# Kernel tuning notes

Hardware: AMD Instinct MI355X
Metric: run time of the kernel (lower is better)

Reference implementation:

```python
import jax, jax.numpy as jnp
import numpy as np

CHANNELS = 512
KSIZE = 5


def conv1d(x, w, b, pad):
    # x: (B, Cin, T), w: (Cout, Cin, k) -> (B, Cout, T)
    y = jax.lax.conv_general_dilated(
        x, w, window_strides=(1,), padding=[(pad, pad)],
        dimension_numbers=('NCH', 'OIH', 'NCH'))
    return y + b[None, :, None]


def setup_inputs() -> dict:
    key = jax.random.key(0)
    ks = jax.random.split(key, 10)
    B, C, T, K = 16, CHANNELS, 2048, KSIZE
    s = 0.02  # conv init scale
    return {
        'x': jax.random.normal(ks[0], (B, C, T), jnp.float32),
        'offset_w': jax.random.normal(ks[1], (2 * K, C, 3), jnp.float32) * s,
        'offset_b': jnp.zeros((2 * K,), jnp.float32),
        'mod_w': jax.random.normal(ks[2], (K, C, 3), jnp.float32) * s,
        'mod_b': jnp.zeros((K,), jnp.float32),
        'weight': jax.random.normal(ks[3], (C, C, K), jnp.float32),
        'rp1_w': jax.random.normal(ks[4], (C // 2, C, 3), jnp.float32) * s,
        'rp1_b': jnp.zeros((C // 2,), jnp.float32),
        'rp2_w': jax.random.normal(ks[5], (1, C // 2, 1), jnp.float32) * s,
        'rp2_b': jnp.zeros((1,), jnp.float32),
    }


def deformable_conv1d(x, offset, modulator, weight):
    B, C, T = x.shape
    K = weight.shape[-1]
    # offset: (B, 2K, T) -> (B, T, 2, K); only component 0 is used (as in torch src)
    off = offset.reshape(B, 2, K, T).transpose(0, 3, 1, 2)[:, :, 0, :]   # (B, T, K)
    mod = modulator.reshape(B, K, T).transpose(0, 2, 1)                   # (B, T, K)
    base = jnp.arange(T, dtype=x.dtype)[None, :, None]
    kpos = (jnp.arange(K, dtype=x.dtype) - K // 2)[None, None, :]
    pos = jnp.clip(base + kpos + off, 0, T - 1)                           # (B, T, K)
    pf = jnp.clip(jnp.floor(pos).astype(jnp.int32), 0, T - 1)
    pc = jnp.clip(jnp.ceil(pos).astype(jnp.int32), 0, T - 1)
    wf = pc.astype(x.dtype) - pos    # NB: both weights are 0 at integer pos (faithful to source)
    wc = pos - pf.astype(x.dtype)
    # gather along time for all channels at once: (B, C, T, K)
    sf = jnp.take_along_axis(x, pf.reshape(B, 1, T * K), axis=2).reshape(B, C, T, K)
    sc = jnp.take_along_axis(x, pc.reshape(B, 1, T * K), axis=2).reshape(B, C, T, K)
    sampled = sf * wf[:, None] + sc * wc[:, None]
    # only diagonal weight[c, c, k] is used in the source loops
    wdiag = weight[jnp.arange(C), jnp.arange(C), :]                       # (C, K)
    return jnp.einsum('bctk,ck,btk->bct', sampled, wdiag, mod)


def reference(x, offset_w, offset_b, mod_w, mod_b, weight, rp1_w, rp1_b, rp2_w, rp2_b):
    offset = conv1d(x, offset_w, offset_b, pad=1)            # (B, 2K, T)
    modulator = jax.nn.sigmoid(conv1d(x, mod_w, mod_b, pad=1))  # (B, K, T)
    deformed = deformable_conv1d(x, offset, modulator, weight)  # (B, C, T)
    h = jax.nn.relu(conv1d(deformed, rp1_w, rp1_b, pad=1))
    strength = conv1d(h, rp2_w, rp2_b, pad=0)[:, 0, :]          # (B, T)
    return deformed, strength
```

## Files before the change

### kernel.cpp

```cpp
#include <hip/hip_runtime.h>
#include <hip/hip_bf16.h>

#define CHN 512
#define TLEN 2048
#define KSZ 5
#define BATCH 16

typedef __hip_bfloat16 bf16;
typedef short bf16x8 __attribute__((ext_vector_type(8)));
typedef float f32x4  __attribute__((ext_vector_type(4)));

#define SAMP_BYTES (BATCH*TLEN*KSZ*8)
#define W1T_ELEMS  (16*4*3*64*40)
#define W1T_BYTES  (W1T_ELEMS*2)
#define WPK_BYTES  65536
#define DT_ROWS    2050
#define DT_CHUNK   (DT_ROWS*32)
#define DT_BYTES   ((size_t)BATCH*16*DT_CHUNK*2)

__global__ __launch_bounds__(256) void kPrep(const float* __restrict__ w1,
    bf16* __restrict__ w1t, const float* __restrict__ ow,
    const float* __restrict__ mw, float* __restrict__ wpk,
    float* __restrict__ outs, const float* __restrict__ b2p,
    bf16* __restrict__ dt)
{
  int bx = blockIdx.x;
  int tidl = threadIdx.x;
  const int NP = W1T_ELEMS/256;
  if (bx < NP) {
    int idx  = bx*256 + tidl;
    int c40  = idx % 40;
    int rest = idx / 40;
    int row  = rest & 63;
    int rr   = rest >> 6;
    int r    = rr % 3;
    int cq   = rr / 3;
    int q    = cq & 3;
    int ch   = cq >> 2;
    int co   = q*64 + row;
    float v = 0.f;
    if (c40 < 32) v = w1[(size_t)co*(CHN*3) + (ch*32 + c40)*3 + r];
    w1t[idx] = __float2bfloat16(v);
  } else if (bx < NP + 64) {
    int idx = (bx - NP)*256 + tidl;
    int j = idx & 31, c = idx >> 5;
    float v = 0.f;
    if (j < 15)      { int o = j/3,  d = j - o*3;  v = ow[o*(CHN*3) + c*3 + d]; }
    else if (j < 30) { int jj = j-15; int o = jj/3, d = jj - o*3;
                       v = mw[o*(CHN*3) + c*3 + d]; }
    wpk[idx] = v;
  } else if (bx < NP + 192) {
    outs[(bx - NP - 64)*256 + tidl] = b2p[0];
  } else if (dt) {
    int z = (bx - NP - 192)*256 + tidl;
    int chunk = z >> 6;
    int row   = ((z >> 5) & 1) ? (DT_ROWS-1) : 0;
    int col   = z & 31;
    dt[(size_t)chunk*DT_CHUNK + row*32 + col] = __float2bfloat16(0.f);
  }
}

__global__ __launch_bounds__(512) void kS(const float* __restrict__ x,
    const float* __restrict__ wpk, const float* __restrict__ ob,
    const float* __restrict__ mb, float2* __restrict__ samp)
{
  int b  = blockIdx.y;
  int t0 = blockIdx.x*64;
  int tx = threadIdx.x;
  int cg = threadIdx.y;
  int t  = t0 + tx;

  __shared__ float red[8][64][10];

  float acc[10];
  #pragma unroll
  for (int i=0;i<10;++i) acc[i]=0.f;
  const float* xb = x + (size_t)b*CHN*TLEN;
  int c0 = cg*64;
  #pragma unroll 4
  for (int c=c0;c<c0+64;++c) {
    int cu = __builtin_amdgcn_readfirstlane(c);
    const float* wp = wpk + cu*32;
    const float* xr = xb + (size_t)cu*TLEN;
    float xm = (t>0)      ? xr[t-1] : 0.f;
    float xc = xr[t];
    float xp = (t<TLEN-1) ? xr[t+1] : 0.f;
    #pragma unroll
    for (int o=0;o<5;++o) {
      acc[o]   = fmaf(xm, wp[o*3+0],    acc[o]);
      acc[o]   = fmaf(xc, wp[o*3+1],    acc[o]);
      acc[o]   = fmaf(xp, wp[o*3+2],    acc[o]);
      acc[5+o] = fmaf(xm, wp[15+o*3+0], acc[5+o]);
      acc[5+o] = fmaf(xc, wp[15+o*3+1], acc[5+o]);
      acc[5+o] = fmaf(xp, wp[15+o*3+2], acc[5+o]);
    }
  }
  #pragma unroll
  for (int i=0;i<10;++i) red[cg][tx][i] = acc[i];
  __syncthreads();
  for (int s=4;s>0;s>>=1) {
    if (cg < s) {
      #pragma unroll
      for (int i=0;i<10;++i) red[cg][tx][i] += red[cg+s][tx][i];
    }
    __syncthreads();
  }
  if (cg==0) {
    #pragma unroll
    for (int k=0;k<KSZ;++k) {
      float off = red[0][tx][k]   + ob[k];
      float mv  = red[0][tx][5+k] + mb[k];
      float sig = 1.f/(1.f + expf(-mv));
      float pos = (float)(t + k - 2) + off;
      pos = fminf(fmaxf(pos, 0.f), (float)(TLEN-1));
      samp[((size_t)b*TLEN + t)*KSZ + k] = make_float2(pos, sig);
    }
  }
}

#define BT   128
#define HALO 16
#define XLEN 160

template<bool WDT>
__global__ __launch_bounds__(256) void kDf(const float* __restrict__ x,
    const float* __restrict__ wgt, const float2* __restrict__ sampg,
    float* __restrict__ out, bf16* __restrict__ dt)
{
  int b  = blockIdx.z;
  int c0 = blockIdx.y*64;
  int t0 = blockIdx.x*BT;
  int tx = threadIdx.x, cy = threadIdx.y;
  int tid = cy*64 + tx;

  __shared__ float  xs[64*XLEN];
  __shared__ float2 sp[BT*KSZ];
  __shared__ int okf;

  int lo = min(max(t0 - HALO, 0), TLEN - XLEN);

  if (tid == 0) okf = 1;
  for (int i = tid; i < BT*KSZ; i += 256)
    sp[i] = sampg[((size_t)b*TLEN + t0)*KSZ + i];

  const float* xb = x + (size_t)b*CHN*TLEN;
  #pragma unroll
  for (int it = 0; it < 10; ++it) {
    int idx = tid + it*256;
    int c  = idx / 40;
    int c4 = idx - c*40;
    const float* src = xb + (size_t)(c0 + c)*TLEN + lo + c4*4;
    __builtin_amdgcn_global_load_lds(
        (const __attribute__((address_space(1))) unsigned int*)src,
        (__attribute__((address_space(3))) unsigned int*)&xs[idx*4],
        16, 0, 0);
  }
  __syncthreads();

  int   bl[2][KSZ];
  float wf[2][KSZ], wc[2][KSZ];
  bool ok = true;
  #pragma unroll
  for (int j=0;j<2;++j)
    #pragma unroll
    for (int k=0;k<KSZ;++k) {
      float2 s = sp[(j*64+tx)*KSZ + k];
      float pos = s.x, sig = s.y;
      float pf = floorf(pos), pc = ceilf(pos);
      int base = min((int)pf, TLEN-2);
      wf[j][k] = (pc - pos)*sig;
      wc[j][k] = (pos - pf)*sig;
      int bloc = base - lo;
      bl[j][k] = bloc;
      ok = ok && (bloc >= 0) && (bloc <= XLEN-2);
    }
  if (!ok) okf = 0;
  __syncthreads();
  int fast = okf;

  unsigned pk0[8], pk1[8];
  if (fast) {
    #pragma unroll
    for (int i=0;i<16;++i) {
      int cl = cy*16 + i;
      int cu = __builtin_amdgcn_readfirstlane(c0 + cl);
      const float* wd = wgt + (size_t)cu*(CHN*KSZ) + (size_t)cu*KSZ;
      float w0 = wd[0], w1v = wd[1], w2v = wd[2], w3 = wd[3], w4 = wd[4];
      const float* xr = xs + cl*XLEN;
      float o0, o1;
      {
        float a = 0.f;
        a = fmaf(fmaf(xr[bl[0][0]+1], wc[0][0], xr[bl[0][0]]*wf[0][0]), w0,  a);
        a = fmaf(fmaf(xr[bl[0][1]+1], wc[0][1], xr[bl[0][1]]*wf[0][1]), w1v, a);
        a = fmaf(fmaf(xr[bl[0][2]+1], wc[0][2], xr[bl[0][2]]*wf[0][2]), w2v, a);
        a = fmaf(fmaf(xr[bl[0][3]+1], wc[0][3], xr[bl[0][3]]*wf[0][3]), w3,  a);
        a = fmaf(fmaf(xr[bl[0][4]+1], wc[0][4], xr[bl[0][4]]*wf[0][4]), w4,  a);
        o0 = a;
      }
      {
        float a = 0.f;
        a = fmaf(fmaf(xr[bl[1][0]+1], wc[1][0], xr[bl[1][0]]*wf[1][0]), w0,  a);
        a = fmaf(fmaf(xr[bl[1][1]+1], wc[1][1], xr[bl[1][1]]*wf[1][1]), w1v, a);
        a = fmaf(fmaf(xr[bl[1][2]+1], wc[1][2], xr[bl[1][2]]*wf[1][2]), w2v, a);
        a = fmaf(fmaf(xr[bl[1][3]+1], wc[1][3], xr[bl[1][3]]*wf[1][3]), w3,  a);
        a = fmaf(fmaf(xr[bl[1][4]+1], wc[1][4], xr[bl[1][4]]*wf[1][4]), w4,  a);
        o1 = a;
      }
      size_t op = ((size_t)b*CHN + cu)*TLEN + t0 + tx;
      out[op]      = o0;
      out[op + 64] = o1;
      if (WDT) {
        union { bf16 h; unsigned short u; } cv0, cv1;
        cv0.h = __float2bfloat16(o0);
        cv1.h = __float2bfloat16(o1);
        if (i & 1) { pk0[i>>1] |= (unsigned)cv0.u << 16;
                     pk1[i>>1] |= (unsigned)cv1.u << 16; }
        else       { pk0[i>>1]  = cv0.u;  pk1[i>>1]  = cv1.u; }
      }
    }
  } else {
    #pragma unroll
    for (int i=0;i<16;++i) {
      int cl = cy*16 + i;
      int cu = __builtin_amdgcn_readfirstlane(c0 + cl);
      const float* wd = wgt + (size_t)cu*(CHN*KSZ) + (size_t)cu*KSZ;
      float wk0 = wd[0], wk1 = wd[1], wk2 = wd[2], wk3 = wd[3], wk4 = wd[4];
      const float* xr = xb + (size_t)cu*TLEN + lo;
      float o[2];
      #pragma unroll
      for (int j=0;j<2;++j) {
        float a = 0.f;
        a = fmaf(fmaf(xr[bl[j][0]+1], wc[j][0], xr[bl[j][0]]*wf[j][0]), wk0, a);
        a = fmaf(fmaf(xr[bl[j][1]+1], wc[j][1], xr[bl[j][1]]*wf[j][1]), wk1, a);
        a = fmaf(fmaf(xr[bl[j][2]+1], wc[j][2], xr[bl[j][2]]*wf[j][2]), wk2, a);
        a = fmaf(fmaf(xr[bl[j][3]+1], wc[j][3], xr[bl[j][3]]*wf[j][3]), wk3, a);
        a = fmaf(fmaf(xr[bl[j][4]+1], wc[j][4], xr[bl[j][4]]*wf[j][4]), wk4, a);
        o[j] = a;
      }
      size_t op = ((size_t)b*CHN + cu)*TLEN + t0 + tx;
      out[op]      = o[0];
      out[op + 64] = o[1];
      if (WDT) {
        union { bf16 h; unsigned short u; } cv0, cv1;
        cv0.h = __float2bfloat16(o[0]);
        cv1.h = __float2bfloat16(o[1]);
        if (i & 1) { pk0[i>>1] |= (unsigned)cv0.u << 16;
                     pk1[i>>1] |= (unsigned)cv1.u << 16; }
        else       { pk0[i>>1]  = cv0.u;  pk1[i>>1]  = cv1.u; }
      }
    }
  }

  if (WDT) {
    int ch   = (c0 >> 5) + (cy >> 1);
    int colb = (cy & 1)*16;
    bf16* p0 = dt + (size_t)(b*16 + ch)*DT_CHUNK
                  + (size_t)(t0 + tx + 1)*32 + colb;
    *(uint4*)p0       = make_uint4(pk0[0], pk0[1], pk0[2], pk0[3]);
    *((uint4*)p0 + 1) = make_uint4(pk0[4], pk0[5], pk0[6], pk0[7]);
    bf16* p1 = p0 + 64*32;
    *(uint4*)p1       = make_uint4(pk1[0], pk1[1], pk1[2], pk1[3]);
    *((uint4*)p1 + 1) = make_uint4(pk1[4], pk1[5], pk1[6], pk1[7]);
  }
}

#define DMA_W2(dst, ch_) do {                                                  \
  const char* gs = (const char*)(w1t + (size_t)((ch_)*4 + m0)*7680);           \
  char* ld = (char*)&Ws[dst][0];                                               \
  for (int of = tid*16; of < 15360; of += 4096) {                              \
    __builtin_amdgcn_global_load_lds(                                          \
        (const __attribute__((address_space(1))) unsigned int*)(gs + of),      \
        (__attribute__((address_space(3))) unsigned int*)(ld + of), 16, 0, 0); \
  }                                                                            \
} while(0)

#define DMA_D2(dst, ch_) do {                                                  \
  const char* gs = (const char*)(dt + (size_t)(b*16 + (ch_))*DT_CHUNK          \
                                    + (size_t)t0*32);                          \
  char* ld = (char*)&Dt[dst][0];                                               \
  for (int of = tid*16; of < 16512; of += 4096) {                              \
    __builtin_amdgcn_global_load_lds(                                          \
        (const __attribute__((address_space(1))) unsigned int*)(gs + of),      \
        (__attribute__((address_space(3))) unsigned int*)(ld + of), 16, 0, 0); \
  }                                                                            \
} while(0)

#define COMPUTE2(cur) do {                                                     \
  _Pragma("unroll")                                                            \
  for (int r=0;r<3;++r) {                                                      \
    bf16x8 af[4], bfr[4];                                                      \
    _Pragma("unroll")                                                          \
    for (int mt=0;mt<4;++mt)                                                   \
      af[mt] = *(const bf16x8*)&Ws[cur][(size_t)(r*64 + mt*16 + ln15)*40 + quad*8];\
    _Pragma("unroll")                                                          \
    for (int nt=0;nt<4;++nt)                                                   \
      bfr[nt] = *(const bf16x8*)&Dt[cur][(size_t)(wN*64 + nt*16 + ln15 + r)*32 + quad*8];\
    _Pragma("unroll")                                                          \
    for (int mt=0;mt<4;++mt)                                                   \
      _Pragma("unroll")                                                        \
      for (int nt=0;nt<4;++nt)                                                 \
        acc[mt][nt] = __builtin_amdgcn_mfma_f32_16x16x32_bf16(                 \
            af[mt], bfr[nt], acc[mt][nt], 0, 0, 0);                            \
  }                                                                            \
} while(0)

__global__ __launch_bounds__(256, 2) void k2d(const bf16* __restrict__ dt,
    const bf16* __restrict__ w1t, const float* __restrict__ b1,
    const float* __restrict__ w2, float* __restrict__ outs)
{
  int n0 = blockIdx.x*256;
  int m0 = blockIdx.y;
  int b  = n0 / TLEN;
  int t0 = n0 % TLEN;
  int tid  = threadIdx.x;
  int lane = tid & 63;
  int wN   = tid >> 6;
  int ln15 = lane & 15, quad = lane >> 4;

  __shared__ bf16 Ws[2][3*64*40];
  __shared__ bf16 Dt[2][258*32];
  __shared__ float Ss[256];

  f32x4 acc[4][4];
  #pragma unroll
  for (int i=0;i<4;++i)
    #pragma unroll
    for (int j=0;j<4;++j) acc[i][j] = (f32x4){0.f,0.f,0.f,0.f};

  DMA_W2(0, 0);
  DMA_D2(0, 0);
  __syncthreads();

  for (int ch=0; ch<16; ++ch) {
    int cur = ch & 1;
    int nxt = cur ^ 1;
    if (ch < 15) {
      DMA_W2(nxt, ch+1);
      DMA_D2(nxt, ch+1);
    }
    COMPUTE2(cur);
    __syncthreads();
  }

  float part[4] = {0.f,0.f,0.f,0.f};
  #pragma unroll
  for (int mt=0;mt<4;++mt) {
    #pragma unroll
    for (int rr=0;rr<4;++rr) {
      int row = m0*64 + mt*16 + quad*4 + rr;
      float bias = b1[row];
      float wv   = w2[row];
      #pragma unroll
      for (int nt=0;nt<4;++nt) {
        float h = acc[mt][nt][rr] + bias;
        h = fmaxf(h, 0.f);
        part[nt] = fmaf(h, wv, part[nt]);
      }
    }
  }
  Ss[tid] = 0.f;
  __syncthreads();
  #pragma unroll
  for (int nt=0;nt<4;++nt)
    atomicAdd(&Ss[wN*64 + nt*16 + ln15], part[nt]);
  __syncthreads();
  atomicAdd(&outs[n0 + tid], Ss[tid]);
}

#define DMA_WSR(dst, ch_) do {                                                 \
  const char* gs = (const char*)(w1t + (size_t)((ch_)*4 + m0)*7680);           \
  char* ld = (char*)&Ws[dst][0];                                               \
  for (int of = tid*16; of < 15360; of += 4096) {                              \
    __builtin_amdgcn_global_load_lds(                                          \
        (const __attribute__((address_space(1))) unsigned int*)(gs + of),      \
        (__attribute__((address_space(3))) unsigned int*)(ld + of), 16, 0, 0); \
  }                                                                            \
} while(0)

#define LOAD_DTR(ch_) do {                                                     \
  const float* dpb = def + ((size_t)b*CHN + (ch_)*32 + g*8)*TLEN;              \
  _Pragma("unroll")                                                            \
  for (int s=0;s<4;++s) {                                                      \
    int t = t0 - 1 + tl + s*64;                                                \
    _Pragma("unroll")                                                          \
    for (int j=0;j<8;++j)                                                      \
      rg[s][j] = (t>=0 && t<TLEN) ? dpb[(size_t)j*TLEN + t] : 0.f;             \
  }                                                                            \
  if (tl < 2) {                                                                \
    int t = t0 - 1 + 256 + tl;                                                 \
    _Pragma("unroll")                                                          \
    for (int j=0;j<8;++j)                                                      \
      rt[j] = (t<TLEN) ? dpb[(size_t)j*TLEN + t] : 0.f;                        \
  }                                                                            \
} while(0)

#define WRITE_DTR(dst) do {                                                    \
  _Pragma("unroll")                                                            \
  for (int s=0;s<4;++s) {                                                      \
    bf16x8 v;                                                                  \
    _Pragma("unroll")                                                          \
    for (int j=0;j<8;++j) { union{bf16 h; short u;} cv;                        \
      cv.h = __float2bfloat16(rg[s][j]); v[j] = cv.u; }                        \
    *(bf16x8*)((char*)&Dt[dst][0] + (tl + s*64)*80 + g*16) = v;                \
  }                                                                            \
  if (tl < 2) {                                                                \
    bf16x8 v;                                                                  \
    _Pragma("unroll")                                                          \
    for (int j=0;j<8;++j) { union{bf16 h; short u;} cv;                        \
      cv.h = __float2bfloat16(rt[j]); v[j] = cv.u; }                           \
    *(bf16x8*)((char*)&Dt[dst][0] + (256 + tl)*80 + g*16) = v;                 \
  }                                                                            \
} while(0)

#define COMPUTER(cur) do {                                                     \
  _Pragma("unroll")                                                            \
  for (int r=0;r<3;++r) {                                                      \
    bf16x8 af[4], bfr[4];                                                      \
    _Pragma("unroll")                                                          \
    for (int mt=0;mt<4;++mt)                                                   \
      af[mt] = *(const bf16x8*)&Ws[cur][(size_t)(r*64 + mt*16 + ln15)*40 + quad*8];\
    _Pragma("unroll")                                                          \
    for (int nt=0;nt<4;++nt)                                                   \
      bfr[nt] = *(const bf16x8*)&Dt[cur][(size_t)(wN*64 + nt*16 + ln15 + r)*40 + quad*8];\
    _Pragma("unroll")                                                          \
    for (int mt=0;mt<4;++mt)                                                   \
      _Pragma("unroll")                                                        \
      for (int nt=0;nt<4;++nt)                                                 \
        acc[mt][nt] = __builtin_amdgcn_mfma_f32_16x16x32_bf16(                 \
            af[mt], bfr[nt], acc[mt][nt], 0, 0, 0);                            \
  }                                                                            \
} while(0)

__global__ __launch_bounds__(256, 2) void k2r(const float* __restrict__ def,
    const bf16* __restrict__ w1t, const float* __restrict__ b1,
    const float* __restrict__ w2, float* __restrict__ outs)
{
  int n0 = blockIdx.x*256;
  int m0 = blockIdx.y;
  int b  = n0 / TLEN;
  int t0 = n0 % TLEN;
  int tid  = threadIdx.x;
  int lane = tid & 63;
  int wN   = tid >> 6;
  int ln15 = lane & 15, quad = lane >> 4;

  __shared__ bf16 Ws[2][3*64*40];
  __shared__ bf16 Dt[2][258*40];
  __shared__ float Ss[256];

  int g  = tid >> 6;
  int tl = tid & 63;

  f32x4 acc[4][4];
  #pragma unroll
  for (int i=0;i<4;++i)
    #pragma unroll
    for (int j=0;j<4;++j) acc[i][j] = (f32x4){0.f,0.f,0.f,0.f};

  float rg[4][8], rt[8];
  #pragma unroll
  for (int j=0;j<8;++j) rt[j] = 0.f;

  DMA_WSR(0, 0);
  LOAD_DTR(0);
  WRITE_DTR(0);
  __syncthreads();

  for (int ch=0; ch<16; ++ch) {
    int cur = ch & 1;
    int nxt = cur ^ 1;
    if (ch < 15) {
      DMA_WSR(nxt, ch+1);
      LOAD_DTR(ch+1);
    }
    COMPUTER(cur);
    if (ch < 15)
      WRITE_DTR(nxt);
    __syncthreads();
  }

  float part[4] = {0.f,0.f,0.f,0.f};
  #pragma unroll
  for (int mt=0;mt<4;++mt) {
    #pragma unroll
    for (int rr=0;rr<4;++rr) {
      int row = m0*64 + mt*16 + quad*4 + rr;
      float bias = b1[row];
      float wv   = w2[row];
      #pragma unroll
      for (int nt=0;nt<4;++nt) {
        float h = acc[mt][nt][rr] + bias;
        h = fmaxf(h, 0.f);
        part[nt] = fmaf(h, wv, part[nt]);
      }
    }
  }
  Ss[tid] = 0.f;
  __syncthreads();
  #pragma unroll
  for (int nt=0;nt<4;++nt)
    atomicAdd(&Ss[wN*64 + nt*16 + ln15], part[nt]);
  __syncthreads();
  atomicAdd(&outs[n0 + tid], Ss[tid]);
}

extern "C" void kernel_launch(void* const* d_in, const int* in_sizes, int n_in,
                              void* d_out, int out_size, void* d_ws, size_t ws_size,
                              hipStream_t stream) {
  const float* x  = (const float*)d_in[0];
  const float* ow = (const float*)d_in[1];
  const float* ob = (const float*)d_in[2];
  const float* mw = (const float*)d_in[3];
  const float* mb = (const float*)d_in[4];
  const float* wg = (const float*)d_in[5];
  const float* w1 = (const float*)d_in[6];
  const float* b1 = (const float*)d_in[7];
  const float* w2 = (const float*)d_in[8];
  const float* b2 = (const float*)d_in[9];

  float* out_def = (float*)d_out;
  float* out_str = out_def + (size_t)BATCH*CHN*TLEN;

  float2* samp = (float2*)d_ws;
  bf16*   w1t  = (bf16*)((char*)d_ws + SAMP_BYTES);
  float*  wpk  = (float*)((char*)d_ws + SAMP_BYTES + W1T_BYTES);

  size_t need = (size_t)SAMP_BYTES + W1T_BYTES + WPK_BYTES + DT_BYTES;
  bf16* dt = (ws_size >= need)
      ? (bf16*)((char*)d_ws + SAMP_BYTES + W1T_BYTES + WPK_BYTES)
      : nullptr;

  kPrep<<<dim3(W1T_ELEMS/256 + 256), 256, 0, stream>>>(
      w1, w1t, ow, mw, wpk, out_str, b2, dt);
  kS   <<<dim3(TLEN/64, BATCH), dim3(64,8), 0, stream>>>(x, wpk, ob, mb, samp);
  if (dt) {
    kDf<true> <<<dim3(TLEN/BT, CHN/64, BATCH), dim3(64,4), 0, stream>>>(
        x, wg, samp, out_def, dt);
    k2d<<<dim3(BATCH*TLEN/256, 4), 256, 0, stream>>>(dt, w1t, b1, w2, out_str);
  } else {
    kDf<false><<<dim3(TLEN/BT, CHN/64, BATCH), dim3(64,4), 0, stream>>>(
        x, wg, samp, out_def, nullptr);
    k2r<<<dim3(BATCH*TLEN/256, 4), 256, 0, stream>>>(out_def, w1t, b1, w2, out_str);
  }
}
```

Before: 214.6 us.

## Shrink deformable kernel to single-wave blocks and drop block barriers

The deformable sampling kernel now runs 64-thread blocks that each handle 16 channels instead of 256-thread blocks over 64 channels. This removes the shared staging of sample positions, the shared fast-path flag and both __syncthreads. Each thread reads its sample data straight from global memory, the fast-path check becomes a wave-wide vote, and an explicit vmcnt wait replaces the barrier for the async LDS loads. Every block now reloads the same sample data, so sample traffic grows fourfold, and the launch uses four times as many small blocks.

```diff
diff --git a/kernel.cpp b/kernel.cpp
--- a/kernel.cpp
+++ b/kernel.cpp
@@ -123,30 +123,23 @@
 #define XLEN 160
 
 template<bool WDT>
-__global__ __launch_bounds__(256) void kDf(const float* __restrict__ x,
+__global__ __launch_bounds__(64) void kDf(const float* __restrict__ x,
     const float* __restrict__ wgt, const float2* __restrict__ sampg,
     float* __restrict__ out, bf16* __restrict__ dt)
 {
   int b  = blockIdx.z;
-  int c0 = blockIdx.y*64;
+  int c0 = blockIdx.y*16;
   int t0 = blockIdx.x*BT;
-  int tx = threadIdx.x, cy = threadIdx.y;
-  int tid = cy*64 + tx;
-
-  __shared__ float  xs[64*XLEN];
-  __shared__ float2 sp[BT*KSZ];
-  __shared__ int okf;
+  int tx = threadIdx.x;
+
+  __shared__ float xs[16*XLEN];
 
   int lo = min(max(t0 - HALO, 0), TLEN - XLEN);
 
-  if (tid == 0) okf = 1;
-  for (int i = tid; i < BT*KSZ; i += 256)
-    sp[i] = sampg[((size_t)b*TLEN + t0)*KSZ + i];
-
   const float* xb = x + (size_t)b*CHN*TLEN;
   #pragma unroll
   for (int it = 0; it < 10; ++it) {
-    int idx = tid + it*256;
+    int idx = tx + it*64;
     int c  = idx / 40;
     int c4 = idx - c*40;
     const float* src = xb + (size_t)(c0 + c)*TLEN + lo + c4*4;
@@ -155,7 +148,6 @@
         (__attribute__((address_space(3))) unsigned int*)&xs[idx*4],
         16, 0, 0);
   }
-  __syncthreads();
 
   int   bl[2][KSZ];
   float wf[2][KSZ], wc[2][KSZ];
@@ -164,7 +156,7 @@
   for (int j=0;j<2;++j)
     #pragma unroll
     for (int k=0;k<KSZ;++k) {
-      float2 s = sp[(j*64+tx)*KSZ + k];
+      float2 s = sampg[((size_t)b*TLEN + t0 + j*64 + tx)*KSZ + k];
       float pos = s.x, sig = s.y;
       float pf = floorf(pos), pc = ceilf(pos);
       int base = min((int)pf, TLEN-2);
@@ -174,19 +166,19 @@
       bl[j][k] = bloc;
       ok = ok && (bloc >= 0) && (bloc <= XLEN-2);
     }
-  if (!ok) okf = 0;
-  __syncthreads();
-  int fast = okf;
+  int fast = __all((int)ok);
+
+  asm volatile("s_waitcnt vmcnt(0)" ::: "memory");
+  __builtin_amdgcn_sched_barrier(0);
 
   unsigned pk0[8], pk1[8];
   if (fast) {
     #pragma unroll
     for (int i=0;i<16;++i) {
-      int cl = cy*16 + i;
-      int cu = __builtin_amdgcn_readfirstlane(c0 + cl);
+      int cu = __builtin_amdgcn_readfirstlane(c0 + i);
       const float* wd = wgt + (size_t)cu*(CHN*KSZ) + (size_t)cu*KSZ;
       float w0 = wd[0], w1v = wd[1], w2v = wd[2], w3 = wd[3], w4 = wd[4];
-      const float* xr = xs + cl*XLEN;
+      const float* xr = xs + i*XLEN;
       float o0, o1;
       {
         float a = 0.f;
@@ -221,8 +213,7 @@
   } else {
     #pragma unroll
     for (int i=0;i<16;++i) {
-      int cl = cy*16 + i;
-      int cu = __builtin_amdgcn_readfirstlane(c0 + cl);
+      int cu = __builtin_amdgcn_readfirstlane(c0 + i);
       const float* wd = wgt + (size_t)cu*(CHN*KSZ) + (size_t)cu*KSZ;
       float wk0 = wd[0], wk1 = wd[1], wk2 = wd[2], wk3 = wd[3], wk4 = wd[4];
       const float* xr = xb + (size_t)cu*TLEN + lo;
@@ -252,8 +243,8 @@
   }
 
   if (WDT) {
-    int ch   = (c0 >> 5) + (cy >> 1);
-    int colb = (cy & 1)*16;
+    int ch   = blockIdx.y >> 1;
+    int colb = (blockIdx.y & 1)*16;
     bf16* p0 = dt + (size_t)(b*16 + ch)*DT_CHUNK
                   + (size_t)(t0 + tx + 1)*32 + colb;
     *(uint4*)p0       = make_uint4(pk0[0], pk0[1], pk0[2], pk0[3]);
@@ -534,11 +525,11 @@
       w1, w1t, ow, mw, wpk, out_str, b2, dt);
   kS   <<<dim3(TLEN/64, BATCH), dim3(64,8), 0, stream>>>(x, wpk, ob, mb, samp);
   if (dt) {
-    kDf<true> <<<dim3(TLEN/BT, CHN/64, BATCH), dim3(64,4), 0, stream>>>(
+    kDf<true> <<<dim3(TLEN/BT, CHN/16, BATCH), 64, 0, stream>>>(
         x, wg, samp, out_def, dt);
     k2d<<<dim3(BATCH*TLEN/256, 4), 256, 0, stream>>>(dt, w1t, b1, w2, out_str);
   } else {
-    kDf<false><<<dim3(TLEN/BT, CHN/64, BATCH), dim3(64,4), 0, stream>>>(
+    kDf<false><<<dim3(TLEN/BT, CHN/16, BATCH), 64, 0, stream>>>(
         x, wg, samp, out_def, nullptr);
     k2r<<<dim3(BATCH*TLEN/256, 4), 256, 0, stream>>>(out_def, w1t, b1, w2, out_str);
   }
```

Result: faster. 209.0 us, median of 2 (-2.6%).
